# Kernel optimization log

Measured on AMD Instinct MI355X. Metric: run time of the kernel, lower is better.

Reference implementation:

```python
import jax, jax.numpy as jnp
import numpy as np

N_NODES = 100000


def _gcn_norm(edge_index, edge_weight, num_nodes):
    # add self-loops with weight 1.0 (PyG GCNConv default)
    loop = jnp.arange(num_nodes, dtype=edge_index.dtype)
    src = jnp.concatenate([edge_index[0], loop])
    dst = jnp.concatenate([edge_index[1], loop])
    ew = jnp.concatenate([edge_weight, jnp.ones((num_nodes,), edge_weight.dtype)])
    deg = jax.ops.segment_sum(ew, dst, num_segments=num_nodes)
    dinv = jnp.where(deg > 0, jax.lax.rsqrt(deg), 0.0)
    norm = dinv[src] * ew * dinv[dst]  # [E + N]
    return src, dst, norm


def _gcn_conv(x, src, dst, norm, W, b):
    h = x @ W                                  # [N, out]
    msg = h[src] * norm[:, None]               # gather + scale
    out = jax.ops.segment_sum(msg, dst, num_segments=x.shape[0])
    return out + b


def setup_inputs() -> dict:
    key = jax.random.key(0)
    ks = jax.random.split(key, 6)
    N, F, H, C, E = N_NODES, 512, 64, 40, 3200000
    x = jax.random.normal(ks[0], (N, F), dtype=jnp.float32)
    edge_index = jax.random.randint(ks[1], (2, E), 0, N, dtype=jnp.int64)
    edge_weight = jax.random.uniform(ks[2], (E,), dtype=jnp.float32)
    W1 = jax.random.normal(ks[3], (F, H), dtype=jnp.float32) * (1.0 / np.sqrt(F))
    b1 = jnp.zeros((H,), jnp.float32)
    W2 = jax.random.normal(ks[4], (H, C), dtype=jnp.float32) * (1.0 / np.sqrt(H))
    b2 = jnp.zeros((C,), jnp.float32)
    return {"x": x, "edge_index": edge_index, "edge_weight": edge_weight,
            "W1": W1, "b1": b1, "W2": W2, "b2": b2}


def reference(x, edge_index, edge_weight, W1, b1, W2, b2):
    src, dst, norm = _gcn_norm(edge_index, edge_weight, x.shape[0])
    h = _gcn_conv(x, src, dst, norm, W1, b1)
    h = jax.nn.relu(h)  # dropout is identity in eval mode
    h = _gcn_conv(h, src, dst, norm, W2, b2)
    return jax.nn.log_softmax(h, axis=1)
```

## Files before the change

kernel.cpp:

```cpp
#include <hip/hip_runtime.h>
#include <math.h>


#define FIN 512
#define FHID 64
#define FOUT 40
#define SCAN_B 1024
#define FIX_SCALE 1073741824.0f
#define FIX_MASK  0xFFFFFFFFFFFFull

typedef unsigned short ushort_t;
typedef unsigned int uint_t;
typedef unsigned long long u64_t;

static __device__ __forceinline__ float bf2f(ushort_t u) {
    return __uint_as_float(((uint_t)u) << 16);
}
static __device__ __forceinline__ ushort_t f2bf(float f) {
    uint_t u = __float_as_uint(f);
    u += 0x7FFFu + ((u >> 16) & 1u);
    return (ushort_t)(u >> 16);
}

__global__ void k_init(u64_t* __restrict__ packed, int n) {
    int i = blockIdx.x * blockDim.x + threadIdx.x;
    if (i < n) packed[i] = (u64_t)1 << 30;
}

__global__ void k_edge_pass1(const int* __restrict__ ei,
                             const float* __restrict__ ew,
                             u64_t* __restrict__ packed, int E) {
    int e = blockIdx.x * blockDim.x + threadIdx.x;
    if (e >= E) return;
    int d = ei[E + e];
    u64_t v = ((u64_t)1 << 48) | (u64_t)(ew[e] * FIX_SCALE + 0.5f);
    atomicAdd(&packed[d], v);
}

__global__ void k_scan1(const u64_t* __restrict__ packed, int* __restrict__ off,
                        int* __restrict__ bsum, int n) {
    __shared__ int s[SCAN_B];
    int tid = threadIdx.x;
    int gid = blockIdx.x * SCAN_B + tid;
    int v = (gid < n) ? (int)(packed[gid] >> 48) : 0;
    s[tid] = v;
    __syncthreads();
    for (int d = 1; d < SCAN_B; d <<= 1) {
        int t = (tid >= d) ? s[tid - d] : 0;
        __syncthreads();
        s[tid] += t;
        __syncthreads();
    }
    if (gid < n) off[gid] = s[tid] - v;
    if (tid == SCAN_B - 1) bsum[blockIdx.x] = s[tid];
}

__global__ void k_scan2(int* __restrict__ bsum, int nb) {
    __shared__ int s[128];
    int tid = threadIdx.x;
    int v = (tid < nb) ? bsum[tid] : 0;
    s[tid] = v;
    __syncthreads();
    for (int d = 1; d < 128; d <<= 1) {
        int t = (tid >= d) ? s[tid - d] : 0;
        __syncthreads();
        s[tid] += t;
        __syncthreads();
    }
    if (tid < nb) bsum[tid] = s[tid] - v;
}

__global__ void k_scan3(int* __restrict__ off, const int* __restrict__ bsum,
                        int* __restrict__ pos, const u64_t* __restrict__ packed,
                        float* __restrict__ dinv, int n) {
    int i = blockIdx.x * blockDim.x + threadIdx.x;
    if (i < n) {
        int o = off[i] + bsum[i / SCAN_B];
        off[i] = o;
        pos[i] = o;
        float deg = (float)(packed[i] & FIX_MASK) * (1.0f / FIX_SCALE);
        dinv[i] = rsqrtf(deg);
    }
}

__global__ void k_scatter(const int* __restrict__ ei, const float* __restrict__ ew,
                          const float* __restrict__ dinv, int* __restrict__ pos,
                          int2* __restrict__ rec, int E) {
    int e = blockIdx.x * blockDim.x + threadIdx.x;
    if (e >= E) return;
    int s = ei[e];
    int d = ei[E + e];
    int p = atomicAdd(&pos[d], 1);
    int2 r;
    r.x = s;
    r.y = __float_as_int(dinv[s] * ew[e] * dinv[d]);
    rec[p] = r;
}

#define G1_MB 32
#define G1_KT 64
__global__ __launch_bounds__(256) void k_gemm1(const float* __restrict__ x,
                                               const float* __restrict__ W,
                                               ushort_t* __restrict__ h, int n) {
    __shared__ float xs[G1_MB][G1_KT];
    int t = threadIdx.x;
    int c = t & 63;
    int g = t >> 6;
    int n0 = blockIdx.x * G1_MB;
    float acc[8];
#pragma unroll
    for (int j = 0; j < 8; ++j) acc[j] = 0.0f;

    int lr = t >> 3;
    int lk = (t & 7) * 8;
    for (int k0 = 0; k0 < FIN; k0 += G1_KT) {
        int node = n0 + lr;
        float4 a = make_float4(0, 0, 0, 0), b = make_float4(0, 0, 0, 0);
        if (node < n) {
            const float* src = &x[(size_t)node * FIN + k0 + lk];
            a = *(const float4*)src;
            b = *(const float4*)(src + 4);
        }
        __syncthreads();
        *(float4*)&xs[lr][lk] = a;
        *(float4*)&xs[lr][lk + 4] = b;
        __syncthreads();
#pragma unroll 4
        for (int q = 0; q < G1_KT; q += 4) {
            float w0 = W[(k0 + q + 0) * FHID + c];
            float w1 = W[(k0 + q + 1) * FHID + c];
            float w2 = W[(k0 + q + 2) * FHID + c];
            float w3 = W[(k0 + q + 3) * FHID + c];
#pragma unroll
            for (int j = 0; j < 8; ++j) {
                float4 xv = *(const float4*)&xs[g * 8 + j][q];
                acc[j] += xv.x * w0 + xv.y * w1 + xv.z * w2 + xv.w * w3;
            }
        }
    }
#pragma unroll
    for (int j = 0; j < 8; ++j) {
        int node = n0 + g * 8 + j;
        if (node < n) h[(size_t)node * FHID + c] = f2bf(acc[j]);
    }
}

__global__ __launch_bounds__(256) void k_agg1(const ushort_t* __restrict__ h1,
                                              const int* __restrict__ off,
                                              const u64_t* __restrict__ packed,
                                              const int2* __restrict__ rec,
                                              const float* __restrict__ dinv,
                                              const float* __restrict__ b1,
                                              ushort_t* __restrict__ z1, int n) {
    int wid = (blockIdx.x * blockDim.x + threadIdx.x) >> 6;
    int lane = threadIdx.x & 63;
    if (wid >= n) return;
    int d = wid;
    float di = dinv[d];
    float acc = di * di * bf2f(h1[(size_t)d * FHID + lane]);
    int start = off[d];
    int m = (int)(packed[d] >> 48);
    int i = 0;
    for (; i + 4 <= m; i += 4) {
        int2 r0 = rec[start + i + 0];
        int2 r1 = rec[start + i + 1];
        int2 r2 = rec[start + i + 2];
        int2 r3 = rec[start + i + 3];
        ushort_t u0 = h1[(size_t)r0.x * FHID + lane];
        ushort_t u1 = h1[(size_t)r1.x * FHID + lane];
        ushort_t u2 = h1[(size_t)r2.x * FHID + lane];
        ushort_t u3 = h1[(size_t)r3.x * FHID + lane];
        acc += __int_as_float(r0.y) * bf2f(u0);
        acc += __int_as_float(r1.y) * bf2f(u1);
        acc += __int_as_float(r2.y) * bf2f(u2);
        acc += __int_as_float(r3.y) * bf2f(u3);
    }
    for (; i < m; ++i) {
        int2 r = rec[start + i];
        acc += __int_as_float(r.y) * bf2f(h1[(size_t)r.x * FHID + lane]);
    }
    acc += b1[lane];
    z1[(size_t)d * FHID + lane] = f2bf(fmaxf(acc, 0.0f));
}

__global__ __launch_bounds__(256) void k_gemm2(const ushort_t* __restrict__ z1,
                                               const float* __restrict__ W2,
                                               ushort_t* __restrict__ h2, int n) {
    __shared__ float ws[FHID * FOUT + 64];
    for (int i = threadIdx.x; i < FHID * FOUT + 64; i += 256)
        ws[i] = (i < FHID * FOUT) ? W2[i] : 0.0f;
    __syncthreads();
    int wid = (blockIdx.x * blockDim.x + threadIdx.x) >> 6;
    int lane = threadIdx.x & 63;
    if (wid >= n) return;
    float v = bf2f(z1[(size_t)wid * FHID + lane]);
    float acc = 0.0f;
#pragma unroll 8
    for (int k = 0; k < FHID; ++k) {
        float zk = __shfl(v, k, 64);
        acc += zk * ws[k * FOUT + lane];
    }
    if (lane < FOUT) h2[(size_t)wid * FOUT + lane] = f2bf(acc);
}

__global__ __launch_bounds__(256) void k_agg2(const ushort_t* __restrict__ h2,
                                              const int* __restrict__ off,
                                              const u64_t* __restrict__ packed,
                                              const int2* __restrict__ rec,
                                              const float* __restrict__ dinv,
                                              const float* __restrict__ b2,
                                              float* __restrict__ out, int n) {
    int wid = (blockIdx.x * blockDim.x + threadIdx.x) >> 6;
    int lane = threadIdx.x & 63;
    if (wid >= n) return;
    int d = wid;
    int cl = (lane < FOUT) ? lane : (FOUT - 1);
    float di = dinv[d];
    float acc = di * di * bf2f(h2[(size_t)d * FOUT + cl]);
    int start = off[d];
    int m = (int)(packed[d] >> 48);
    int i = 0;
    for (; i + 4 <= m; i += 4) {
        int2 r0 = rec[start + i + 0];
        int2 r1 = rec[start + i + 1];
        int2 r2 = rec[start + i + 2];
        int2 r3 = rec[start + i + 3];
        ushort_t u0 = h2[(size_t)r0.x * FOUT + cl];
        ushort_t u1 = h2[(size_t)r1.x * FOUT + cl];
        ushort_t u2 = h2[(size_t)r2.x * FOUT + cl];
        ushort_t u3 = h2[(size_t)r3.x * FOUT + cl];
        acc += __int_as_float(r0.y) * bf2f(u0);
        acc += __int_as_float(r1.y) * bf2f(u1);
        acc += __int_as_float(r2.y) * bf2f(u2);
        acc += __int_as_float(r3.y) * bf2f(u3);
    }
    for (; i < m; ++i) {
        int2 r = rec[start + i];
        acc += __int_as_float(r.y) * bf2f(h2[(size_t)r.x * FOUT + cl]);
    }
    acc += b2[cl];
    float mv = (lane < FOUT) ? acc : -INFINITY;
#pragma unroll
    for (int o = 32; o > 0; o >>= 1) mv = fmaxf(mv, __shfl_xor(mv, o, 64));
    float ex = (lane < FOUT) ? expf(acc - mv) : 0.0f;
    float ssum = ex;
#pragma unroll
    for (int o = 32; o > 0; o >>= 1) ssum += __shfl_xor(ssum, o, 64);
    if (lane < FOUT) out[(size_t)d * FOUT + lane] = acc - mv - logf(ssum);
}

extern "C" void kernel_launch(void* const* d_in, const int* in_sizes, int n_in,
                              void* d_out, int out_size, void* d_ws, size_t ws_size,
                              hipStream_t stream) {
    const float* x   = (const float*)d_in[0];
    const int*   ei  = (const int*)d_in[1];
    const float* ew  = (const float*)d_in[2];
    const float* W1  = (const float*)d_in[3];
    const float* b1  = (const float*)d_in[4];
    const float* W2  = (const float*)d_in[5];
    const float* b2  = (const float*)d_in[6];
    float* out       = (float*)d_out;

    const int N = in_sizes[0] / FIN;
    const int E = in_sizes[2];

    char* w = (char*)d_ws;
    auto alloc = [&](size_t bytes) -> char* {
        char* p = w;
        w += (bytes + 255) & ~(size_t)255;
        return p;
    };
    u64_t*    packed = (u64_t*)alloc((size_t)N * 8);
    float*    dinv   = (float*)alloc((size_t)N * 4);
    int*      off    = (int*)  alloc((size_t)N * 4);
    int*      pos    = (int*)  alloc((size_t)N * 4);
    int*      bsum   = (int*)  alloc(((N + SCAN_B - 1) / SCAN_B) * 4);
    int2*     rec    = (int2*) alloc((size_t)E * 8);
    ushort_t* h1     = (ushort_t*)alloc((size_t)N * FHID * 2);
    ushort_t* z1     = (ushort_t*)alloc((size_t)N * FHID * 2);
    ushort_t* h2     = (ushort_t*)alloc((size_t)N * FOUT * 2);
    (void)ws_size; (void)n_in; (void)out_size;

    k_init<<<(N + 255) / 256, 256, 0, stream>>>(packed, N);
    k_edge_pass1<<<(E + 255) / 256, 256, 0, stream>>>(ei, ew, packed, E);
    int nb = (N + SCAN_B - 1) / SCAN_B;
    k_scan1<<<nb, SCAN_B, 0, stream>>>(packed, off, bsum, N);
    k_scan2<<<1, 128, 0, stream>>>(bsum, nb);
    k_scan3<<<(N + 255) / 256, 256, 0, stream>>>(off, bsum, pos, packed, dinv, N);
    k_scatter<<<(E + 255) / 256, 256, 0, stream>>>(ei, ew, dinv, pos, rec, E);
    k_gemm1<<<(N + G1_MB - 1) / G1_MB, 256, 0, stream>>>(x, W1, h1, N);
    k_agg1<<<(N + 3) / 4, 256, 0, stream>>>(h1, off, packed, rec, dinv, b1, z1, N);
    k_gemm2<<<(N + 3) / 4, 256, 0, stream>>>(z1, W2, h2, N);
    k_agg2<<<(N + 3) / 4, 256, 0, stream>>>(h2, off, packed, rec, dinv, b2, out, N);
}
```

Baseline: 1.046 ms.

## Compute first-layer GEMM with bf16 MFMA using pre-transposed bf16 weights

Replaces the FP32 shared-memory tiled x@W1 kernel with one where each wavefront computes a 16x64 output tile using 16x16x32 bf16 MFMA instructions. A new small kernel converts W1 to bf16 and transposes it once per call. x is converted to bf16 in registers while loading, which lowers input precision. The aim is to cut the compute cost of the 100000x512x64 GEMM so it becomes bound by streaming x from memory. There is no tail guard beyond row0<n, so N must be a multiple of 16.

```diff
diff --git a/kernel.cpp b/kernel.cpp
--- a/kernel.cpp
+++ b/kernel.cpp
@@ -12,6 +12,8 @@
 typedef unsigned short ushort_t;
 typedef unsigned int uint_t;
 typedef unsigned long long u64_t;
+typedef __attribute__((ext_vector_type(8))) short bf16x8;
+typedef __attribute__((ext_vector_type(4))) float f32x4;
 
 static __device__ __forceinline__ float bf2f(ushort_t u) {
     return __uint_as_float(((uint_t)u) << 16);
@@ -97,51 +99,51 @@
     rec[p] = r;
 }
 
-#define G1_MB 32
-#define G1_KT 64
+__global__ void k_convW1(const float* __restrict__ W, ushort_t* __restrict__ Wt) {
+    int idx = blockIdx.x * blockDim.x + threadIdx.x;
+    int c = idx >> 9;
+    int k = idx & 511;
+    Wt[idx] = f2bf(W[k * FHID + c]);
+}
+
 __global__ __launch_bounds__(256) void k_gemm1(const float* __restrict__ x,
-                                               const float* __restrict__ W,
+                                               const ushort_t* __restrict__ Wt,
                                                ushort_t* __restrict__ h, int n) {
-    __shared__ float xs[G1_MB][G1_KT];
     int t = threadIdx.x;
-    int c = t & 63;
-    int g = t >> 6;
-    int n0 = blockIdx.x * G1_MB;
-    float acc[8];
+    int lane = t & 63;
+    int wv = t >> 6;
+    int row0 = blockIdx.x * 64 + wv * 16;
+    if (row0 >= n) return;
+    int r = lane & 15;
+    int kg = lane >> 4;
+    int koff = kg * 8;
+    const float* xrow = x + (size_t)(row0 + r) * FIN;
+    const ushort_t* wbase = Wt + (size_t)r * FIN + koff;
+    f32x4 acc0 = {0,0,0,0}, acc1 = {0,0,0,0}, acc2 = {0,0,0,0}, acc3 = {0,0,0,0};
+    for (int k0 = 0; k0 < FIN; k0 += 32) {
+        float4 a0 = *(const float4*)(xrow + k0 + koff);
+        float4 a1 = *(const float4*)(xrow + k0 + koff + 4);
+        bf16x8 af;
+        af[0] = (short)f2bf(a0.x); af[1] = (short)f2bf(a0.y);
+        af[2] = (short)f2bf(a0.z); af[3] = (short)f2bf(a0.w);
+        af[4] = (short)f2bf(a1.x); af[5] = (short)f2bf(a1.y);
+        af[6] = (short)f2bf(a1.z); af[7] = (short)f2bf(a1.w);
+        bf16x8 b0 = *(const bf16x8*)(wbase + k0);
+        bf16x8 b1 = *(const bf16x8*)(wbase + k0 + 16 * FIN);
+        bf16x8 b2 = *(const bf16x8*)(wbase + k0 + 32 * FIN);
+        bf16x8 b3 = *(const bf16x8*)(wbase + k0 + 48 * FIN);
+        acc0 = __builtin_amdgcn_mfma_f32_16x16x32_bf16(af, b0, acc0, 0, 0, 0);
+        acc1 = __builtin_amdgcn_mfma_f32_16x16x32_bf16(af, b1, acc1, 0, 0, 0);
+        acc2 = __builtin_amdgcn_mfma_f32_16x16x32_bf16(af, b2, acc2, 0, 0, 0);
+        acc3 = __builtin_amdgcn_mfma_f32_16x16x32_bf16(af, b3, acc3, 0, 0, 0);
+    }
+    ushort_t* hb = h + (size_t)(row0 + kg * 4) * FHID + r;
 #pragma unroll
-    for (int j = 0; j < 8; ++j) acc[j] = 0.0f;
-
-    int lr = t >> 3;
-    int lk = (t & 7) * 8;
-    for (int k0 = 0; k0 < FIN; k0 += G1_KT) {
-        int node = n0 + lr;
-        float4 a = make_float4(0, 0, 0, 0), b = make_float4(0, 0, 0, 0);
-        if (node < n) {
-            const float* src = &x[(size_t)node * FIN + k0 + lk];
-            a = *(const float4*)src;
-            b = *(const float4*)(src + 4);
-        }
-        __syncthreads();
-        *(float4*)&xs[lr][lk] = a;
-        *(float4*)&xs[lr][lk + 4] = b;
-        __syncthreads();
-#pragma unroll 4
-        for (int q = 0; q < G1_KT; q += 4) {
-            float w0 = W[(k0 + q + 0) * FHID + c];
-            float w1 = W[(k0 + q + 1) * FHID + c];
-            float w2 = W[(k0 + q + 2) * FHID + c];
-            float w3 = W[(k0 + q + 3) * FHID + c];
-#pragma unroll
-            for (int j = 0; j < 8; ++j) {
-                float4 xv = *(const float4*)&xs[g * 8 + j][q];
-                acc[j] += xv.x * w0 + xv.y * w1 + xv.z * w2 + xv.w * w3;
-            }
-        }
-    }
-#pragma unroll
-    for (int j = 0; j < 8; ++j) {
-        int node = n0 + g * 8 + j;
-        if (node < n) h[(size_t)node * FHID + c] = f2bf(acc[j]);
+    for (int j = 0; j < 4; ++j) {
+        hb[(size_t)j * FHID +  0] = f2bf(acc0[j]);
+        hb[(size_t)j * FHID + 16] = f2bf(acc1[j]);
+        hb[(size_t)j * FHID + 32] = f2bf(acc2[j]);
+        hb[(size_t)j * FHID + 48] = f2bf(acc3[j]);
     }
 }
 
@@ -276,6 +278,7 @@
     int*      pos    = (int*)  alloc((size_t)N * 4);
     int*      bsum   = (int*)  alloc(((N + SCAN_B - 1) / SCAN_B) * 4);
     int2*     rec    = (int2*) alloc((size_t)E * 8);
+    ushort_t* Wt     = (ushort_t*)alloc((size_t)FHID * FIN * 2);
     ushort_t* h1     = (ushort_t*)alloc((size_t)N * FHID * 2);
     ushort_t* z1     = (ushort_t*)alloc((size_t)N * FHID * 2);
     ushort_t* h2     = (ushort_t*)alloc((size_t)N * FOUT * 2);
@@ -288,7 +291,8 @@
     k_scan2<<<1, 128, 0, stream>>>(bsum, nb);
     k_scan3<<<(N + 255) / 256, 256, 0, stream>>>(off, bsum, pos, packed, dinv, N);
     k_scatter<<<(E + 255) / 256, 256, 0, stream>>>(ei, ew, dinv, pos, rec, E);
-    k_gemm1<<<(N + G1_MB - 1) / G1_MB, 256, 0, stream>>>(x, W1, h1, N);
+    k_convW1<<<(FHID * FIN) / 256, 256, 0, stream>>>(W1, Wt);
+    k_gemm1<<<(N + 63) / 64, 256, 0, stream>>>(x, Wt, h1, N);
     k_agg1<<<(N + 3) / 4, 256, 0, stream>>>(h1, off, packed, rec, dinv, b1, z1, N);
     k_gemm2<<<(N + 3) / 4, 256, 0, stream>>>(z1, W2, h2, N);
     k_agg2<<<(N + 3) / 4, 256, 0, stream>>>(h2, off, packed, rec, dinv, b2, out, N);
```

After: 936.6 us. 10.4% less time.
